# Performance work log

Measured on AMD Instinct MI355X. Metric: run time of the kernel, lower is better.

Reference implementation:

```python
import jax, jax.numpy as jnp
import numpy as np
from jax import lax

N, CIN, COUT, H, W = 16, 512, 256, 32, 32
EPS = 1e-5


def _conv(x, w, b, pad_h, pad_w):
    # x: [N,Cin,H,W], w: [Cout,Cin,kh,kw], pad = ((top,bottom),(left,right))
    y = lax.conv_general_dilated(
        x, w, window_strides=(1, 1), padding=(pad_h, pad_w),
        dimension_numbers=("NCHW", "OIHW", "NCHW"))
    return y + b[None, :, None, None]


def setup_inputs() -> dict:
    key = jax.random.key(0)
    ks = jax.random.split(key, 12)
    s = 0.02
    return {
        "x": jax.random.normal(ks[0], (N, CIN, H, W), jnp.float32),
        "w1": jax.random.normal(ks[1], (COUT, CIN, 3, 3), jnp.float32) * s,
        "b1": jax.random.normal(ks[2], (COUT,), jnp.float32) * s,
        "w2": jax.random.normal(ks[3], (COUT, CIN, 2, 3), jnp.float32) * s,
        "b2": jax.random.normal(ks[4], (COUT,), jnp.float32) * s,
        "w3": jax.random.normal(ks[5], (COUT, CIN, 3, 2), jnp.float32) * s,
        "b3": jax.random.normal(ks[6], (COUT,), jnp.float32) * s,
        "w4": jax.random.normal(ks[7], (COUT, CIN, 2, 2), jnp.float32) * s,
        "b4": jax.random.normal(ks[8], (COUT,), jnp.float32) * s,
        "gamma": jnp.ones((COUT,), jnp.float32),
        "beta": jnp.zeros((COUT,), jnp.float32),
    }


def reference(x, w1, b1, w2, b2, w3, b3, w4, b4, gamma, beta):
    # torch F.pad(l,r,t,b) -> lax padding ((top,bottom),(left,right))
    o1 = _conv(x, w1, b1, (1, 1), (1, 1))  # 3x3, pad (1,1,1,1) -> [N,Cout,H,W]
    o2 = _conv(x, w2, b2, (1, 0), (1, 1))  # 2x3, pad (1,1,1,0)
    o3 = _conv(x, w3, b3, (1, 1), (1, 0))  # 3x2, pad (1,0,1,1)
    o4 = _conv(x, w4, b4, (1, 0), (1, 0))  # 2x2, pad (1,0,1,0)
    # pixel-shuffle interleave: o1->(even,even), o2->(odd,even), o3->(even,odd), o4->(odd,odd)
    row_even = jnp.stack([o1, o3], axis=-1).reshape(N, COUT, H, 2 * W)
    row_odd = jnp.stack([o2, o4], axis=-1).reshape(N, COUT, H, 2 * W)
    y = jnp.stack([row_even, row_odd], axis=-2).reshape(N, COUT, 2 * H, 2 * W)
    # BatchNorm2d, training mode: biased batch stats over (N,H,W)
    mean = jnp.mean(y, axis=(0, 2, 3), keepdims=True)
    var = jnp.mean(jnp.square(y - mean), axis=(0, 2, 3), keepdims=True)
    normed = (y - mean) * lax.rsqrt(var + EPS)
    normed = normed * gamma[None, :, None, None] + beta[None, :, None, None]
    return jax.nn.relu(normed)
```

## Files before the change

kernel.cpp:

```cpp
#include <hip/hip_runtime.h>
#include <hip/hip_bf16.h>


typedef unsigned short ushort_t;
typedef __attribute__((ext_vector_type(8))) short short8;
typedef __attribute__((ext_vector_type(4))) float floatx4;
typedef __attribute__((ext_vector_type(2))) float floatx2;
typedef __attribute__((ext_vector_type(4))) unsigned short u16x4;
typedef __attribute__((ext_vector_type(8))) unsigned short u16x8;
typedef __attribute__((ext_vector_type(4))) unsigned int u32x4;

#define XT_OFF    0u
#define WT_OFF    18939904u
#define BIAS_OFF  28377088u
#define STATS_OFF 28381184u

#define NSITES 204

#define ASYNC16(g, l) __builtin_amdgcn_global_load_lds( \
    (const __attribute__((address_space(1))) void*)(g), \
    (__attribute__((address_space(3))) void*)(l), 16, 0, 0)

__device__ __forceinline__ ushort_t f2bf(float f) {
  unsigned int u = __builtin_bit_cast(unsigned int, f);
  u += 0x7fffu + ((u >> 16) & 1u);
  return (ushort_t)(u >> 16);
}

__global__ __launch_bounds__(256) void prep_x(const float* __restrict__ x,
                                              ushort_t* __restrict__ xt) {
  const int b = blockIdx.x;
  const int n = b / 34, hp = b % 34;
  const int t = threadIdx.x;
  ushort_t* dst = xt + (size_t)(n * 34 + hp) * (34 * 512);
  if (hp == 0 || hp == 33) {
    u32x4 z = {0u, 0u, 0u, 0u};
    for (int i = t; i < 2176; i += 256) ((u32x4*)dst)[i] = z;
    return;
  }
  const int h = hp - 1;
  {
    u32x4 z = {0u, 0u, 0u, 0u};
    if (t < 64) ((u32x4*)dst)[t] = z;
    else if (t < 128) ((u32x4*)(dst + 33 * 512))[t - 64] = z;
  }
  __shared__ ushort_t lds[128 * 36];
  const size_t base = (size_t)n * 524288 + (size_t)h * 32;
  for (int ci0 = 0; ci0 < 512; ci0 += 128) {
    __syncthreads();
    {
      const int cil = t >> 3;
      const int w4 = (t & 7) << 2;
#pragma unroll
      for (int cc = 0; cc < 4; ++cc) {
        const int ci = cil + cc * 32;
        floatx4 v = *(const floatx4*)(x + base + (size_t)(ci0 + ci) * 1024 + w4);
        u16x4 hv;
#pragma unroll
        for (int j = 0; j < 4; ++j) hv[j] = f2bf(v[j]);
        *(u16x4*)&lds[ci * 36 + w4] = hv;
      }
    }
    __syncthreads();
    {
      const int w = t & 31;
      const int j8 = t >> 5;
#pragma unroll
      for (int cc2 = 0; cc2 < 2; ++cc2) {
        const int cil = cc2 * 64 + j8 * 8;
        u16x8 v;
#pragma unroll
        for (int j = 0; j < 8; ++j) v[j] = lds[(cil + j) * 36 + w];
        *(u16x8*)(dst + (w + 1) * 512 + ci0 + cil) = v;
      }
    }
  }
}

__global__ __launch_bounds__(256) void prep_w(
    const float* __restrict__ w1, const float* __restrict__ w2,
    const float* __restrict__ w3, const float* __restrict__ w4,
    const float* __restrict__ b1, const float* __restrict__ b2,
    const float* __restrict__ b3, const float* __restrict__ b4,
    ushort_t* __restrict__ wt, float* __restrict__ bias) {
  const int nout = blockIdx.x;
  const int q = nout >> 8, co = nout & 255;
  const int row = ((q & 1) << 9) + (co << 1) + (q >> 1);
  const int t = threadIdx.x;
  const float* wsrc; const float* bsrc; int khl, kwl;
  if (q == 0)      { wsrc = w1; bsrc = b1; khl = 3; kwl = 3; }
  else if (q == 1) { wsrc = w2; bsrc = b2; khl = 2; kwl = 3; }
  else if (q == 2) { wsrc = w3; bsrc = b3; khl = 3; kwl = 2; }
  else             { wsrc = w4; bsrc = b4; khl = 2; kwl = 2; }
  if (t == 0) bias[row] = bsrc[co];
  ushort_t* dst = wt + (size_t)row * 4608;
  for (int tap = 0; tap < 9; ++tap) {
    const int dh = tap / 3, dw = tap % 3;
    const bool valid = (dh < khl) && (dw < kwl);
#pragma unroll
    for (int cc = 0; cc < 2; ++cc) {
      const int ci = cc * 256 + t;
      ushort_t v = 0;
      if (valid) v = f2bf(wsrc[(((size_t)co * 512 + ci) * khl + dh) * kwl + dw]);
      dst[tap * 512 + ci] = v;
    }
  }
}

__global__ void zero_stats(float* __restrict__ stats) {
  stats[threadIdx.x] = 0.f;
}

template <int NTAPS>
__device__ __forceinline__ void gemm_body(
    const ushort_t* __restrict__ xt, const ushort_t* __restrict__ wt,
    const float* __restrict__ bias, float* __restrict__ out,
    float* __restrict__ stats, char* ldsX, char* ldsW0, char* ldsW1) {
  const int tid = threadIdx.x;
  const int bx = blockIdx.x;
  const int bn = bx & 7, bm = bx >> 3;
  const int n0 = bn << 7;
  const int n_img = bm >> 3;
  const int h0p = (bm & 7) << 2;
  const int wv = tid >> 6, lane = tid & 63;
  const int ri = lane & 15, kg = lane >> 4;
  const int wm = (wv & 1) << 6, wn = (wv >> 1) << 6;

  const char* xgp[7];
  char* xlp[7];
  {
    const char* xg = (const char*)(xt + (size_t)(n_img * 34 + h0p) * (34 * 512));
#pragma unroll
    for (int p = 0; p < 7; ++p) {
      const int idx = p * 256 + tid;
      const int site = idx >> 3, slot = idx & 7;
      const int c = slot ^ (site & 7);
      xgp[p] = xg + site * 1024 + (c << 4);
      xlp[p] = ldsX + idx * 16;
    }
  }
  const char* wgp[4];
  char* wlp0[4];
  char* wlp1[4];
#pragma unroll
  for (int p = 0; p < 4; ++p) {
    const int idx = p * 256 + tid;
    const int row = idx >> 3, slot = idx & 7;
    const int c = slot ^ (row & 7);
    wgp[p] = (const char*)wt + (size_t)(n0 + row) * 9216 + (c << 4);
    wlp0[p] = ldsW0 + idx * 16;
    wlp1[p] = ldsW1 + idx * 16;
  }

  floatx4 acc[4][4] = {};

  int arow[4], bsite[4];
#pragma unroll
  for (int f = 0; f < 4; ++f) arow[f] = wn + (f << 4) + ri;
#pragma unroll
  for (int fj = 0; fj < 4; ++fj)
    bsite[fj] = ((wm >> 5) + (fj >> 1)) * 34 + ((fj & 1) << 4) + ri;

  for (int chunk = 0; chunk < 8; ++chunk) {
    const int cb = chunk << 7;
#pragma unroll
    for (int p = 0; p < 6; ++p) ASYNC16(xgp[p] + cb, xlp[p]);
    if (tid < 96) ASYNC16(xgp[6] + cb, xlp[6]);
#pragma unroll
    for (int p = 0; p < 4; ++p) ASYNC16(wgp[p] + cb, wlp0[p]);
    __syncthreads();
#pragma unroll
    for (int tap = 0; tap < NTAPS; ++tap) {
      if (tap + 1 < NTAPS) {
        const int noff = ((tap + 1) << 10) + cb;
        if (tap & 1) {
#pragma unroll
          for (int p = 0; p < 4; ++p) ASYNC16(wgp[p] + noff, wlp0[p]);
        } else {
#pragma unroll
          for (int p = 0; p < 4; ++p) ASYNC16(wgp[p] + noff, wlp1[p]);
        }
      }
      const char* wb = (tap & 1) ? ldsW1 : ldsW0;
      const int tsite = (tap / 3) * 34 + (tap % 3);
#pragma unroll
      for (int ks = 0; ks < 2; ++ks) {
        const int c = (ks << 2) + kg;
        short8 a4[4], b4[4];
#pragma unroll
        for (int f = 0; f < 4; ++f)
          a4[f] = *(const short8*)(wb + arow[f] * 128 +
                                   ((c ^ (arow[f] & 7)) << 4));
#pragma unroll
        for (int fj = 0; fj < 4; ++fj) {
          const int srow = bsite[fj] + tsite;
          b4[fj] = *(const short8*)(ldsX + srow * 128 + ((c ^ (srow & 7)) << 4));
        }
#pragma unroll
        for (int fi = 0; fi < 4; ++fi)
#pragma unroll
          for (int fj = 0; fj < 4; ++fj)
            acc[fi][fj] = __builtin_amdgcn_mfma_f32_16x16x32_bf16(
                a4[fi], b4[fj], acc[fi][fj], 0, 0, 0);
      }
      __syncthreads();
    }
  }

  const int quad = kg, colL = ri;
  const int dh6 = (bn >> 2) << 6;
#pragma unroll
  for (int fi = 0; fi < 4; ++fi) {
    const int rbase = n0 + wn + (fi << 4) + (quad << 2);
    const floatx4 bv = *(const floatx4*)(bias + rbase);
    const int co = (rbase & 511) >> 1;
    float sA = 0.f, s2A = 0.f, sB = 0.f, s2B = 0.f;
    float* ob = out + (((size_t)(n_img * 256 + co)) << 12) + dh6;
#pragma unroll
    for (int fj = 0; fj < 4; ++fj) {
      const int mb = wm + (fj << 4) + colL;
      const int h = h0p + (mb >> 5), w = mb & 31;
      const float v0 = acc[fi][fj][0] + bv[0];
      const float v1 = acc[fi][fj][1] + bv[1];
      const float v2 = acc[fi][fj][2] + bv[2];
      const float v3 = acc[fi][fj][3] + bv[3];
      sA += v0 + v1;
      s2A += v0 * v0 + v1 * v1;
      sB += v2 + v3;
      s2B += v2 * v2 + v3 * v3;
      float* p = ob + (h << 7) + (w << 1);
      floatx2 eA = {v0, v1};
      floatx2 eB = {v2, v3};
      *(floatx2*)p = eA;
      *(floatx2*)(p + 4096) = eB;
    }
#pragma unroll
    for (int off = 1; off < 16; off <<= 1) {
      sA += __shfl_xor(sA, off);
      s2A += __shfl_xor(s2A, off);
      sB += __shfl_xor(sB, off);
      s2B += __shfl_xor(s2B, off);
    }
    if (colL == 0) {
      atomicAdd(&stats[co], sA);
      atomicAdd(&stats[256 + co], s2A);
      atomicAdd(&stats[co + 1], sB);
      atomicAdd(&stats[256 + co + 1], s2B);
    }
  }
}

__global__ __launch_bounds__(256) void gemm_kernel(
    const ushort_t* __restrict__ xt, const ushort_t* __restrict__ wt,
    const float* __restrict__ bias, float* __restrict__ out,
    float* __restrict__ stats) {
  __shared__ char ldsX[NSITES * 128];
  __shared__ char ldsW[2][128 * 128];
  if ((blockIdx.x & 7) < 4)
    gemm_body<9>(xt, wt, bias, out, stats, ldsX, ldsW[0], ldsW[1]);
  else
    gemm_body<6>(xt, wt, bias, out, stats, ldsX, ldsW[0], ldsW[1]);
}

__global__ __launch_bounds__(256) void bn_apply(
    float* __restrict__ y, const float* __restrict__ stats,
    const float* __restrict__ gamma, const float* __restrict__ beta) {
  const int b = blockIdx.x;
  const int co = b & 255;
  const int t = threadIdx.x;
  const float mean = stats[co] * (1.f / 65536.f);
  const float var = stats[256 + co] * (1.f / 65536.f) - mean * mean;
  const float rstd = rsqrtf(var + 1e-5f);
  const float scale = rstd * gamma[co];
  const float shift = beta[co] - mean * scale;
  float* p = y + (size_t)b * 4096;
#pragma unroll
  for (int it = 0; it < 4; ++it) {
    floatx4* q = (floatx4*)(p + (it * 256 + t) * 4);
    floatx4 v = *q;
#pragma unroll
    for (int e = 0; e < 4; ++e) v[e] = fmaxf(v[e] * scale + shift, 0.f);
    *q = v;
  }
}

extern "C" void kernel_launch(void* const* d_in, const int* in_sizes, int n_in,
                              void* d_out, int out_size, void* d_ws,
                              size_t ws_size, hipStream_t stream) {
  const float* x  = (const float*)d_in[0];
  const float* w1 = (const float*)d_in[1];
  const float* b1 = (const float*)d_in[2];
  const float* w2 = (const float*)d_in[3];
  const float* b2 = (const float*)d_in[4];
  const float* w3 = (const float*)d_in[5];
  const float* b3 = (const float*)d_in[6];
  const float* w4 = (const float*)d_in[7];
  const float* b4 = (const float*)d_in[8];
  const float* gamma = (const float*)d_in[9];
  const float* beta  = (const float*)d_in[10];
  float* out = (float*)d_out;

  char* ws = (char*)d_ws;
  ushort_t* xt   = (ushort_t*)(ws + XT_OFF);
  ushort_t* wt   = (ushort_t*)(ws + WT_OFF);
  float*    bias = (float*)(ws + BIAS_OFF);
  float*    st   = (float*)(ws + STATS_OFF);

  zero_stats<<<1, 512, 0, stream>>>(st);
  prep_x<<<16 * 34, 256, 0, stream>>>(x, xt);
  prep_w<<<1024, 256, 0, stream>>>(w1, w2, w3, w4, b1, b2, b3, b4, wt, bias);
  gemm_kernel<<<1024, 256, 0, stream>>>(xt, wt, bias, out, st);
  bn_apply<<<4096, 256, 0, stream>>>(out, st, gamma, beta);
}
```

Measured before the change: 280.1 us.

## Double GEMM M-tile to 256 output sites per block and fold stats zeroing into prep_w

Result: slower. 454.0 us (+62.1%).

```diff
diff --git a/kernel.cpp b/kernel.cpp
--- a/kernel.cpp
+++ b/kernel.cpp
@@ -15,7 +15,7 @@
 #define BIAS_OFF  28377088u
 #define STATS_OFF 28381184u
 
-#define NSITES 204
+#define NSITES 340
 
 #define ASYNC16(g, l) __builtin_amdgcn_global_load_lds( \
     (const __attribute__((address_space(1))) void*)(g), \
@@ -82,11 +82,13 @@
     const float* __restrict__ w3, const float* __restrict__ w4,
     const float* __restrict__ b1, const float* __restrict__ b2,
     const float* __restrict__ b3, const float* __restrict__ b4,
-    ushort_t* __restrict__ wt, float* __restrict__ bias) {
+    ushort_t* __restrict__ wt, float* __restrict__ bias,
+    float* __restrict__ stats) {
   const int nout = blockIdx.x;
   const int q = nout >> 8, co = nout & 255;
   const int row = ((q & 1) << 9) + (co << 1) + (q >> 1);
   const int t = threadIdx.x;
+  if (nout == 0) { stats[t] = 0.f; stats[t + 256] = 0.f; }
   const float* wsrc; const float* bsrc; int khl, kwl;
   if (q == 0)      { wsrc = w1; bsrc = b1; khl = 3; kwl = 3; }
   else if (q == 1) { wsrc = w2; bsrc = b2; khl = 2; kwl = 3; }
@@ -107,67 +109,46 @@
   }
 }
 
-__global__ void zero_stats(float* __restrict__ stats) {
-  stats[threadIdx.x] = 0.f;
-}
-
 template <int NTAPS>
 __device__ __forceinline__ void gemm_body(
     const ushort_t* __restrict__ xt, const ushort_t* __restrict__ wt,
     const float* __restrict__ bias, float* __restrict__ out,
-    float* __restrict__ stats, char* ldsX, char* ldsW0, char* ldsW1) {
+    float* __restrict__ stats, char* ldsX, char* ldsW0, char* ldsW1,
+    int bn, int bm) {
   const int tid = threadIdx.x;
-  const int bx = blockIdx.x;
-  const int bn = bx & 7, bm = bx >> 3;
   const int n0 = bn << 7;
-  const int n_img = bm >> 3;
-  const int h0p = (bm & 7) << 2;
+  const int n_img = bm >> 2;
+  const int h0p = (bm & 3) << 3;
   const int wv = tid >> 6, lane = tid & 63;
   const int ri = lane & 15, kg = lane >> 4;
-  const int wm = (wv & 1) << 6, wn = (wv >> 1) << 6;
-
-  const char* xgp[7];
-  char* xlp[7];
-  {
-    const char* xg = (const char*)(xt + (size_t)(n_img * 34 + h0p) * (34 * 512));
-#pragma unroll
-    for (int p = 0; p < 7; ++p) {
-      const int idx = p * 256 + tid;
-      const int site = idx >> 3, slot = idx & 7;
-      const int c = slot ^ (site & 7);
-      xgp[p] = xg + site * 1024 + (c << 4);
-      xlp[p] = ldsX + idx * 16;
-    }
-  }
-  const char* wgp[4];
-  char* wlp0[4];
-  char* wlp1[4];
-#pragma unroll
-  for (int p = 0; p < 4; ++p) {
-    const int idx = p * 256 + tid;
-    const int row = idx >> 3, slot = idx & 7;
-    const int c = slot ^ (row & 7);
-    wgp[p] = (const char*)wt + (size_t)(n0 + row) * 9216 + (c << 4);
-    wlp0[p] = ldsW0 + idx * 16;
-    wlp1[p] = ldsW1 + idx * 16;
-  }
-
-  floatx4 acc[4][4] = {};
-
-  int arow[4], bsite[4];
+  const int wm = (wv & 1) << 7, wn = (wv >> 1) << 6;
+
+  const int slot = tid & 7;
+  const int site0 = tid >> 3;
+  const int cs = slot ^ (site0 & 7);
+  const char* xgb = (const char*)(xt + (size_t)(n_img * 34 + h0p) * (34 * 512))
+                    + site0 * 1024 + (cs << 4);
+  char* xlb = ldsX + tid * 16;
+  const char* wgb = (const char*)wt + (size_t)(n0 + site0) * 9216 + (cs << 4);
+  char* wlb0 = ldsW0 + tid * 16;
+  char* wlb1 = ldsW1 + tid * 16;
+
+  floatx4 acc[4][8] = {};
+
+  int arow[4], bsite[8];
 #pragma unroll
   for (int f = 0; f < 4; ++f) arow[f] = wn + (f << 4) + ri;
 #pragma unroll
-  for (int fj = 0; fj < 4; ++fj)
+  for (int fj = 0; fj < 8; ++fj)
     bsite[fj] = ((wm >> 5) + (fj >> 1)) * 34 + ((fj & 1) << 4) + ri;
 
   for (int chunk = 0; chunk < 8; ++chunk) {
     const int cb = chunk << 7;
 #pragma unroll
-    for (int p = 0; p < 6; ++p) ASYNC16(xgp[p] + cb, xlp[p]);
-    if (tid < 96) ASYNC16(xgp[6] + cb, xlp[6]);
-#pragma unroll
-    for (int p = 0; p < 4; ++p) ASYNC16(wgp[p] + cb, wlp0[p]);
+    for (int p = 0; p < 10; ++p) ASYNC16(xgb + p * 32768 + cb, xlb + p * 4096);
+    if (tid < 160) ASYNC16(xgb + 327680 + cb, xlb + 40960);
+#pragma unroll
+    for (int p = 0; p < 4; ++p) ASYNC16(wgb + p * 294912 + cb, wlb0 + p * 4096);
     __syncthreads();
 #pragma unroll
     for (int tap = 0; tap < NTAPS; ++tap) {
@@ -175,10 +156,12 @@
         const int noff = ((tap + 1) << 10) + cb;
         if (tap & 1) {
 #pragma unroll
-          for (int p = 0; p < 4; ++p) ASYNC16(wgp[p] + noff, wlp0[p]);
+          for (int p = 0; p < 4; ++p)
+            ASYNC16(wgb + p * 294912 + noff, wlb0 + p * 4096);
         } else {
 #pragma unroll
-          for (int p = 0; p < 4; ++p) ASYNC16(wgp[p] + noff, wlp1[p]);
+          for (int p = 0; p < 4; ++p)
+            ASYNC16(wgb + p * 294912 + noff, wlb1 + p * 4096);
         }
       }
       const char* wb = (tap & 1) ? ldsW1 : ldsW0;
@@ -186,20 +169,20 @@
 #pragma unroll
       for (int ks = 0; ks < 2; ++ks) {
         const int c = (ks << 2) + kg;
-        short8 a4[4], b4[4];
+        short8 a4[4], b4[8];
 #pragma unroll
         for (int f = 0; f < 4; ++f)
           a4[f] = *(const short8*)(wb + arow[f] * 128 +
                                    ((c ^ (arow[f] & 7)) << 4));
 #pragma unroll
-        for (int fj = 0; fj < 4; ++fj) {
+        for (int fj = 0; fj < 8; ++fj) {
           const int srow = bsite[fj] + tsite;
           b4[fj] = *(const short8*)(ldsX + srow * 128 + ((c ^ (srow & 7)) << 4));
         }
 #pragma unroll
         for (int fi = 0; fi < 4; ++fi)
 #pragma unroll
-          for (int fj = 0; fj < 4; ++fj)
+          for (int fj = 0; fj < 8; ++fj)
             acc[fi][fj] = __builtin_amdgcn_mfma_f32_16x16x32_bf16(
                 a4[fi], b4[fj], acc[fi][fj], 0, 0, 0);
       }
@@ -217,7 +200,7 @@
     float sA = 0.f, s2A = 0.f, sB = 0.f, s2B = 0.f;
     float* ob = out + (((size_t)(n_img * 256 + co)) << 12) + dh6;
 #pragma unroll
-    for (int fj = 0; fj < 4; ++fj) {
+    for (int fj = 0; fj < 8; ++fj) {
       const int mb = wm + (fj << 4) + colL;
       const int h = h0p + (mb >> 5), w = mb & 31;
       const float v0 = acc[fi][fj][0] + bv[0];
@@ -250,16 +233,19 @@
   }
 }
 
-__global__ __launch_bounds__(256) void gemm_kernel(
+__global__ __launch_bounds__(256, 2) void gemm_kernel(
     const ushort_t* __restrict__ xt, const ushort_t* __restrict__ wt,
     const float* __restrict__ bias, float* __restrict__ out,
     float* __restrict__ stats) {
   __shared__ char ldsX[NSITES * 128];
   __shared__ char ldsW[2][128 * 128];
-  if ((blockIdx.x & 7) < 4)
-    gemm_body<9>(xt, wt, bias, out, stats, ldsX, ldsW[0], ldsW[1]);
+  const int bx = blockIdx.x;
+  const int bn = (bx & 7) ^ (((bx >> 8) & 1) << 2);
+  const int bm = (bx >> 3) & 63;
+  if (bn < 4)
+    gemm_body<9>(xt, wt, bias, out, stats, ldsX, ldsW[0], ldsW[1], bn, bm);
   else
-    gemm_body<6>(xt, wt, bias, out, stats, ldsX, ldsW[0], ldsW[1]);
+    gemm_body<6>(xt, wt, bias, out, stats, ldsX, ldsW[0], ldsW[1], bn, bm);
 }
 
 __global__ __launch_bounds__(256) void bn_apply(
@@ -306,9 +292,8 @@
   float*    bias = (float*)(ws + BIAS_OFF);
   float*    st   = (float*)(ws + STATS_OFF);
 
-  zero_stats<<<1, 512, 0, stream>>>(st);
   prep_x<<<16 * 34, 256, 0, stream>>>(x, xt);
-  prep_w<<<1024, 256, 0, stream>>>(w1, w2, w3, w4, b1, b2, b3, b4, wt, bias);
-  gemm_kernel<<<1024, 256, 0, stream>>>(xt, wt, bias, out, st);
+  prep_w<<<1024, 256, 0, stream>>>(w1, w2, w3, w4, b1, b2, b3, b4, wt, bias, st);
+  gemm_kernel<<<512, 256, 0, stream>>>(xt, wt, bias, out, st);
   bn_apply<<<4096, 256, 0, stream>>>(out, st, gamma, beta);
 }
```
